# Kernel optimization log

Hardware: AMD Instinct MI355X
Metric: run time of the kernel (lower is better)

The kernel has to match this reference:

```python
import jax, jax.numpy as jnp
import numpy as np

N = 100000      # num nodes (single ntype)
D_IN = 256      # input_dim
D_OUT = 128     # output_dim (embedding_dim)
H = 4           # attn_heads
C = D_OUT // H  # out_channels per head
R = 3           # num metapaths with tail 'gene'; num_tail_relations = R + 1
E = 600000      # edges per metapath


def setup_inputs() -> dict:
    key = jax.random.key(0)
    ks = jax.random.split(key, 12)
    x = jax.random.normal(ks[0], (N, D_IN), dtype=jnp.float32)
    edge_index = jax.random.randint(ks[1], (R, 2, E), 0, N, dtype=jnp.int32)
    # per-ntype linear_l / linear_r (single ntype 'gene')
    sc = 1.0 / np.sqrt(D_IN)
    Wl = jax.random.normal(ks[2], (D_IN, D_OUT), dtype=jnp.float32) * sc
    bl = jnp.zeros((D_OUT,), dtype=jnp.float32)
    Wr = jax.random.normal(ks[3], (D_IN, D_OUT), dtype=jnp.float32) * sc
    br = jnp.zeros((D_OUT,), dtype=jnp.float32)
    # edge-level attention params: (R, H, 2C)
    attn = jax.random.normal(ks[4], (R, H, 2 * C), dtype=jnp.float32) * 0.1
    # relation-level attention params
    rel_attn_l = jax.random.normal(ks[5], (H, C), dtype=jnp.float32) * 0.1
    rel_attn_r = jax.random.normal(ks[6], (R + 1, H, C), dtype=jnp.float32) * 0.1
    rel_bias = jnp.zeros((R + 1,), dtype=jnp.float32)
    return {"x": x, "edge_index": edge_index, "Wl": Wl, "bl": bl, "Wr": Wr,
            "br": br, "attn": attn, "rel_attn_l": rel_attn_l,
            "rel_attn_r": rel_attn_r, "rel_bias": rel_bias}


def _segment_softmax(logits, seg, num_segments):
    # logits: (E, H), seg: (E,) dst ids -> softmax over edges sharing a dst
    m = jax.ops.segment_max(logits, seg, num_segments=num_segments)  # (N, H)
    e = jnp.exp(logits - m[seg])
    s = jax.ops.segment_sum(e, seg, num_segments=num_segments)       # (N, H)
    return e / (s[seg] + 1e-16)


def reference(x, edge_index, Wl, bl, Wr, br, attn, rel_attn_l, rel_attn_r, rel_bias):
    # projection: relu(Linear(x)).view(N, H, C)
    l = jax.nn.relu(x @ Wl + bl).reshape(N, H, C)
    r = jax.nn.relu(x @ Wr + br).reshape(N, H, C)

    def per_relation(ei, attn_m):
        src, dst = ei[0], ei[1]
        # alpha_e = LeakyReLU( l[src].attn_l + r[dst].attn_r ), per head
        a = (jnp.einsum('ehc,hc->eh', l[src], attn_m[:, :C])
             + jnp.einsum('ehc,hc->eh', r[dst], attn_m[:, C:]))  # (E, H)
        a = jax.nn.leaky_relu(a, negative_slope=0.2)
        alpha = _segment_softmax(a, dst, N)                      # (E, H)
        msg = l[src] * alpha[..., None]                          # (E, H, C)
        return jax.ops.segment_sum(msg, dst, num_segments=N)     # (N, H, C)

    emb_rel = jax.vmap(per_relation)(edge_index, attn)           # (R, N, H, C)
    # last relation slot is the self projection l
    emb = jnp.concatenate([jnp.moveaxis(emb_rel, 0, 1), l[:, None]], axis=1)  # (N, R+1, H, C)

    # relation-level beta attention
    beta_l = jax.nn.relu(r * rel_attn_l)                          # (N, H, C)
    beta_r = jax.nn.relu(emb * rel_attn_r)                        # (N, R+1, H, C)
    beta = jnp.einsum('nhc,nrhc->nrh', beta_l, beta_r) + rel_bias[None, :, None]
    beta = jax.nn.softmax(beta, axis=1)                           # (N, R+1, H)

    h = (emb * beta[..., None]).sum(axis=1).reshape(N, D_OUT)
    return jax.nn.relu(h)
```

## Files before the change

kernel.cpp:

```cpp
#include <hip/hip_runtime.h>
#include <hip/hip_bf16.h>

#define N_NODES 100000
#define N_EDGES 600000
#define N_REL   3
#define D_INF   256
#define D_OUTF  128
#define TOT_E   (3 * N_EDGES)

#define NB_REL   49
#define NBUCKT   (3 * NB_REL)
#define CAPB     16384

#define NPART_BLOCKS ((TOT_E + 4095) / 4096)

#define NPROJ_BLOCKS (((N_NODES + 63) / 64) * 2)
#define NTOT_BLOCKS  (NPROJ_BLOCKS + NBUCKT)

typedef __attribute__((ext_vector_type(8))) short          bf16x8;
typedef __attribute__((ext_vector_type(8))) unsigned short ushort8;
typedef __attribute__((ext_vector_type(4))) float          f32x4;

#define LPAD 72
#define LTS  136

__device__ __forceinline__ unsigned short bf16_rne(float v) {
    unsigned int b = __float_as_uint(v);
    b += 0x7FFFu + ((b >> 16) & 1u);
    return (unsigned short)(b >> 16);
}

__global__ __launch_bounds__(256) void part_wt(
    const float* __restrict__ Wl, const float* __restrict__ Wr,
    unsigned short* __restrict__ wt,
    const int* __restrict__ ei, int* __restrict__ bcnt,
    uint2* __restrict__ gstage)
{
    const int bid = blockIdx.x;
    const int t   = threadIdx.x;
    if (bid < 256) {
        const int k = bid;
        const int w = t >> 7;
        const int n = t & 127;
        const float v = (w ? Wr : Wl)[(size_t)k * D_OUTF + n];
        const unsigned short h = bf16_rne(v);
        const float fhi = __uint_as_float(((unsigned int)h) << 16);
        const unsigned short g = bf16_rne(v - fhi);
        const int kb   = k >> 6;
        const int kk   = (k >> 5) & 1;
        const int lgrp = (k >> 3) & 3;
        const int j    = k & 7;
        const int cf   = n >> 4;
        const int lane = lgrp * 16 + (n & 15);
        const size_t fh = ((((size_t)(w * 2 + 0) * 4 + kb) * 2 + kk) * 8 + cf) * 512 + lane * 8 + j;
        const size_t fl = ((((size_t)(w * 2 + 1) * 4 + kb) * 2 + kk) * 8 + cf) * 512 + lane * 8 + j;
        wt[fh] = h;
        wt[fl] = g;
        return;
    }
    __shared__ int lh[NBUCKT];
    __shared__ int lc[NBUCKT];
    const int base = (bid - 256) * 4096;

    for (int q = t; q < NBUCKT; q += 256) lh[q] = 0;
    __syncthreads();
#pragma unroll
    for (int r = 0; r < 16; ++r) {
        const int ge = base + r * 256 + t;
        if (ge < TOT_E) {
            const int rr = (ge >= 2 * N_EDGES) ? 2 : ((ge >= N_EDGES) ? 1 : 0);
            const int e  = ge - rr * N_EDGES;
            const int dst = ei[(size_t)rr * 2 * N_EDGES + N_EDGES + e];
            atomicAdd(&lh[rr * NB_REL + (dst >> 11)], 1);
        }
    }
    __syncthreads();
    for (int q = t; q < NBUCKT; q += 256)
        lc[q] = lh[q] ? atomicAdd(&bcnt[q], lh[q]) : 0;
    __syncthreads();
#pragma unroll
    for (int r = 0; r < 16; ++r) {
        const int ge = base + r * 256 + t;
        if (ge < TOT_E) {
            const int rr = (ge >= 2 * N_EDGES) ? 2 : ((ge >= N_EDGES) ? 1 : 0);
            const int e  = ge - rr * N_EDGES;
            const int src = ei[(size_t)rr * 2 * N_EDGES + e];
            const int dst = ei[(size_t)rr * 2 * N_EDGES + N_EDGES + e];
            const int qb  = rr * NB_REL + (dst >> 11);
            const int off = atomicAdd(&lc[qb], 1);
            uint2 u; u.x = (unsigned)src; u.y = (unsigned)(dst | (rr << 20));
            gstage[(size_t)qb * CAPB + off] = u;
        }
    }
}

__global__ __launch_bounds__(256, 6) void proj_scatter(
    const float* __restrict__ x, const unsigned short* __restrict__ wt,
    const float* __restrict__ bl, const float* __restrict__ br,
    const float* __restrict__ attn,
    float* __restrict__ rbuf,
    float* __restrict__ alr,  float* __restrict__ ar,
    unsigned short* __restrict__ lbf,
    const uint2* __restrict__ gstage, const int* __restrict__ bcnt,
    int* __restrict__ deg, int* __restrict__ rowst, int* __restrict__ colall)
{
    __shared__ unsigned short smem[2 * 64 * LPAD];
    __shared__ int wsum2[4];
    __shared__ int wexcl2[4];

    const int bid = blockIdx.x;
    const unsigned int pb = (unsigned int)(((unsigned long long)bid * NPROJ_BLOCKS) / NTOT_BLOCKS);
    const unsigned int pa = (unsigned int)(((unsigned long long)(bid + 1) * NPROJ_BLOCKS) / NTOT_BLOCKS);

    if (pa == pb) {
        const int b     = bid - (int)pb;
        const int rrb   = b / NB_REL;
        const int node0 = (b % NB_REL) * 2048;
        const int nN    = min(2048, N_NODES - node0);
        const int t     = threadIdx.x;
        int* hist = (int*)smem;
        const int cnt_b = bcnt[b];
        const size_t sbase = (size_t)b * CAPB;

        {
            int pv = (t < b) ? bcnt[t] : 0;
#pragma unroll
            for (int m = 32; m >= 1; m >>= 1) pv += __shfl_xor(pv, m);
            if ((t & 63) == 0) wsum2[t >> 6] = pv;
        }
        for (int q = t; q < 2048; q += 256) hist[q] = 0;
        __syncthreads();
        const int gb = wsum2[0] + wsum2[1] + wsum2[2] + wsum2[3];

        for (int e = t; e < cnt_b; e += 256) {
            const uint2 u = gstage[sbase + e];
            atomicAdd(&hist[(int)(u.y & 0xFFFFFu) - node0], 1);
        }
        __syncthreads();
        for (int q = t; q < nN; q += 256)
            deg[rrb * N_NODES + node0 + q] = hist[q];
        __syncthreads();
        {
            const int lane = t & 63;
            const int wid  = t >> 6;
            int v[8]; int tsum = 0;
#pragma unroll
            for (int i = 0; i < 8; ++i) { v[i] = hist[t * 8 + i]; tsum += v[i]; }
            int inc = tsum;
#pragma unroll
            for (int off2 = 1; off2 < 64; off2 <<= 1) {
                const int u2 = __shfl_up(inc, off2);
                if (lane >= off2) inc += u2;
            }
            if (lane == 63) wsum2[wid] = inc;
            __syncthreads();
            if (t == 0) {
                int s = 0;
#pragma unroll
                for (int i2 = 0; i2 < 4; ++i2) { const int tv = wsum2[i2]; wexcl2[i2] = s; s += tv; }
            }
            __syncthreads();
            int run = gb + wexcl2[wid] + (inc - tsum);
#pragma unroll
            for (int i = 0; i < 8; ++i) {
                const int q = t * 8 + i;
                const int st = run;
                run += v[i];
                hist[q] = st;
                if (q < nN) rowst[rrb * N_NODES + node0 + q] = st;
            }
        }
        __syncthreads();
        for (int e = t; e < cnt_b; e += 256) {
            const uint2 u = gstage[sbase + e];
            const int loc = (int)(u.y & 0xFFFFFu) - node0;
            const int pos = atomicAdd(&hist[loc], 1);
            colall[pos] = (int)u.x;
        }
        return;
    }

    const int tid  = threadIdx.x;
    const int nb   = (int)(pb >> 1) * 64;
    const int w    = (int)(pb & 1);

    const int lane = tid & 63;
    const int wv   = tid >> 6;
    const int rowf = lane & 15;
    const int kgrp = lane >> 4;

    f32x4 acc[8];
#pragma unroll
    for (int cf = 0; cf < 8; ++cf) acc[cf] = (f32x4){0.f, 0.f, 0.f, 0.f};

    for (int kb4 = 0; kb4 < 4; ++kb4) {
        __syncthreads();
        {
            const int r   = tid >> 2;
            const int seg = tid & 3;
            int rowg = nb + r; if (rowg >= N_NODES) rowg = N_NODES - 1;
            const float* src = x + (size_t)rowg * D_INF + kb4 * 64 + seg * 16;
#pragma unroll
            for (int q2 = 0; q2 < 2; ++q2) {
                const float4 v0 = *reinterpret_cast<const float4*>(src + q2 * 8);
                const float4 v1 = *reinterpret_cast<const float4*>(src + q2 * 8 + 4);
                const float vv[8] = {v0.x, v0.y, v0.z, v0.w, v1.x, v1.y, v1.z, v1.w};
                ushort8 hv, gv;
#pragma unroll
                for (int q = 0; q < 8; ++q) {
                    const unsigned short h = bf16_rne(vv[q]);
                    hv[q] = h;
                    const float fhi = __uint_as_float(((unsigned int)h) << 16);
                    gv[q] = bf16_rne(vv[q] - fhi);
                }
                *reinterpret_cast<ushort8*>(&smem[0 * 64 * LPAD + r * LPAD + seg * 16 + q2 * 8]) = hv;
                *reinterpret_cast<ushort8*>(&smem[1 * 64 * LPAD + r * LPAD + seg * 16 + q2 * 8]) = gv;
            }
        }
        __syncthreads();

#pragma unroll
        for (int kk = 0; kk < 2; ++kk) {
            const int ko = kk * 32 + kgrp * 8;
            const bf16x8 ahi = *reinterpret_cast<const bf16x8*>(&smem[0 * 64 * LPAD + (wv * 16 + rowf) * LPAD + ko]);
            const bf16x8 alo = *reinterpret_cast<const bf16x8*>(&smem[1 * 64 * LPAD + (wv * 16 + rowf) * LPAD + ko]);
#pragma unroll
            for (int cf = 0; cf < 8; ++cf) {
                const bf16x8 bhi = *reinterpret_cast<const bf16x8*>(
                    wt + ((((size_t)(w * 2 + 0) * 4 + kb4) * 2 + kk) * 8 + cf) * 512 + lane * 8);
                const bf16x8 blo = *reinterpret_cast<const bf16x8*>(
                    wt + ((((size_t)(w * 2 + 1) * 4 + kb4) * 2 + kk) * 8 + cf) * 512 + lane * 8);
                acc[cf] = __builtin_amdgcn_mfma_f32_16x16x32_bf16(ahi, bhi, acc[cf], 0, 0, 0);
                acc[cf] = __builtin_amdgcn_mfma_f32_16x16x32_bf16(ahi, blo, acc[cf], 0, 0, 0);
                acc[cf] = __builtin_amdgcn_mfma_f32_16x16x32_bf16(alo, bhi, acc[cf], 0, 0, 0);
            }
        }
    }
    __syncthreads();

    float o_[8][4];
    {
        const float* bias = w ? br : bl;
#pragma unroll
        for (int cf = 0; cf < 8; ++cf) {
            const float bvv = bias[cf * 16 + rowf];
#pragma unroll
            for (int j = 0; j < 4; ++j)
                o_[cf][j] = fmaxf(acc[cf][j] + bvv, 0.f);
        }
    }

    if (w == 1) {
#pragma unroll
        for (int cf = 0; cf < 8; ++cf)
#pragma unroll
            for (int j = 0; j < 4; ++j) {
                const int node = nb + wv * 16 + kgrp * 4 + j;
                if (node < N_NODES)
                    rbuf[(size_t)node * D_OUTF + cf * 16 + rowf] = o_[cf][j];
            }
    }

    {
        const int woff = w ? 32 : 0;
#pragma unroll
        for (int rr = 0; rr < 3; ++rr) {
            float pr[4][4];
#pragma unroll
            for (int hh = 0; hh < 4; ++hh) {
                const float A0 = attn[rr * 256 + hh * 64 + woff + rowf];
                const float A1 = attn[rr * 256 + hh * 64 + woff + 16 + rowf];
#pragma unroll
                for (int j = 0; j < 4; ++j)
                    pr[hh][j] = fmaf(o_[2 * hh][j], A0, o_[2 * hh + 1][j] * A1);
            }
#pragma unroll
            for (int hh = 0; hh < 4; ++hh)
#pragma unroll
                for (int j = 0; j < 4; ++j) {
#pragma unroll
                    for (int m = 8; m >= 1; m >>= 1)
                        pr[hh][j] += __shfl_xor(pr[hh][j], m);
                }
            if ((rowf >> 2) == rr) {
#pragma unroll
                for (int j = 0; j < 4; ++j) {
                    float v = pr[0][j];
#pragma unroll
                    for (int hh = 1; hh < 4; ++hh)
                        if ((rowf & 3) == hh) v = pr[hh][j];
                    const int node = nb + wv * 16 + kgrp * 4 + j;
                    if (node < N_NODES) {
                        if (w == 0)
                            alr[((size_t)rr * N_NODES + node) * 4 + (rowf & 3)] = v;
                        else
                            ar[(size_t)node * 12 + rowf] = v;
                    }
                }
            }
        }
    }

    if (w == 0) {
#pragma unroll
        for (int cf = 0; cf < 8; ++cf)
#pragma unroll
            for (int j = 0; j < 4; ++j)
                smem[(wv * 16 + kgrp * 4 + j) * LTS + cf * 16 + rowf] = bf16_rne(o_[cf][j]);
        __syncthreads();
#pragma unroll
        for (int q = 0; q < 4; ++q) {
            const int idx = tid + q * 256;
            const int r2  = idx >> 4;
            const int c8  = (idx & 15) * 8;
            const int node = nb + r2;
            if (node < N_NODES)
                *reinterpret_cast<ushort8*>(&lbf[(size_t)node * D_OUTF + c8]) =
                    *reinterpret_cast<ushort8*>(&smem[r2 * LTS + c8]);
        }
    }
}

__global__ __launch_bounds__(256) void aggregate_kernel(
    const uint4* __restrict__ lbf128, const float* __restrict__ rbuf,
    const float* __restrict__ alr,  const float* __restrict__ ar,
    const int* __restrict__ rowst,  const int* __restrict__ deg,
    const int* __restrict__ colall,
    const float* __restrict__ rel_attn_l, const float* __restrict__ rel_attn_r,
    const float* __restrict__ rel_bias,   float* __restrict__ out)
{
    __shared__ int   src_sh[4][4][3][16];
    __shared__ float w_sh[4][4][3][16][4];

    const int wv   = threadIdx.x >> 6;
    const int lane = threadIdx.x & 63;
    const int g    = lane >> 4;
    const int j    = lane & 15;
    const int n    = blockIdx.x * 16 + wv * 4 + g;

    const int h  = j >> 2;
    const int c8 = j * 8;

    int   start_[3], cnt_[3], cm_[3], base_[3];
    float4 ar4_[3];
#pragma unroll
    for (int rr = 0; rr < 3; ++rr) {
        start_[rr] = rowst[rr * N_NODES + n];
        cnt_[rr]   = deg[rr * N_NODES + n];
        ar4_[rr]   = *reinterpret_cast<const float4*>(ar + (size_t)n * 12 + rr * 4);
        int cm = cnt_[rr];
        cm = max(cm, __shfl_xor(cm, 16));
        cm = max(cm, __shfl_xor(cm, 32));
        cm_[rr] = cm;
        base_[rr] = 0;
    }

    float ex[3][8];
    float den[3];
#pragma unroll
    for (int rr = 0; rr < 3; ++rr) {
        den[rr] = 0.f;
#pragma unroll
        for (int c = 0; c < 8; ++c) ex[rr][c] = 0.f;
    }

    while (base_[0] < cm_[0] || base_[1] < cm_[1] || base_[2] < cm_[2]) {
        int mm_[3];
        int mxw_[3];
#pragma unroll
        for (int rr = 0; rr < 3; ++rr) {
            mm_[rr] = 0; mxw_[rr] = 0;
            if (base_[rr] < cm_[rr]) {
                mm_[rr]  = min(16, max(0, cnt_[rr] - base_[rr]));
                mxw_[rr] = min(16, cm_[rr] - base_[rr]);
                const int sj = (j < mm_[rr]) ? colall[start_[rr] + base_[rr] + j] : 0;
                const float4 al4 = *reinterpret_cast<const float4*>(
                    alr + ((size_t)rr * N_NODES + sj) * 4);
                float t0 = al4.x + ar4_[rr].x, t1 = al4.y + ar4_[rr].y;
                float t2 = al4.z + ar4_[rr].z, t3 = al4.w + ar4_[rr].w;
                t0 = fmaxf(t0, 0.2f * t0); t1 = fmaxf(t1, 0.2f * t1);
                t2 = fmaxf(t2, 0.2f * t2); t3 = fmaxf(t3, 0.2f * t3);
                float e0 = __expf(t0), e1 = __expf(t1);
                float e2 = __expf(t2), e3 = __expf(t3);
                if (j >= mm_[rr]) { e0 = 0.f; e1 = 0.f; e2 = 0.f; e3 = 0.f; }
                src_sh[wv][g][rr][j] = sj;
                f32x4 w4; w4[0] = e0; w4[1] = e1; w4[2] = e2; w4[3] = e3;
                *reinterpret_cast<f32x4*>(&w_sh[wv][g][rr][j][0]) = w4;
            }
        }
        const int mxall = max(mxw_[0], max(mxw_[1], mxw_[2]));
        for (int i = 0; i < mxall; ++i) {
#pragma unroll
            for (int rr = 0; rr < 3; ++rr) {
                if (i < mm_[rr]) {
                    const int   srcI = src_sh[wv][g][rr][i];
                    const float wsel = w_sh[wv][g][rr][i][h];
                    const uint4 u = lbf128[(size_t)srcI * 16 + j];
                    den[rr] += wsel;
                    ex[rr][0] = fmaf(wsel, __uint_as_float(u.x << 16),         ex[rr][0]);
                    ex[rr][1] = fmaf(wsel, __uint_as_float(u.x & 0xFFFF0000u), ex[rr][1]);
                    ex[rr][2] = fmaf(wsel, __uint_as_float(u.y << 16),         ex[rr][2]);
                    ex[rr][3] = fmaf(wsel, __uint_as_float(u.y & 0xFFFF0000u), ex[rr][3]);
                    ex[rr][4] = fmaf(wsel, __uint_as_float(u.z << 16),         ex[rr][4]);
                    ex[rr][5] = fmaf(wsel, __uint_as_float(u.z & 0xFFFF0000u), ex[rr][5]);
                    ex[rr][6] = fmaf(wsel, __uint_as_float(u.w << 16),         ex[rr][6]);
                    ex[rr][7] = fmaf(wsel, __uint_as_float(u.w & 0xFFFF0000u), ex[rr][7]);
                }
            }
        }
#pragma unroll
        for (int rr = 0; rr < 3; ++rr) base_[rr] += 16;
    }

    float e[4][8];
#pragma unroll
    for (int rr = 0; rr < 3; ++rr) {
        const float inv = 1.f / (den[rr] + 1e-16f);
#pragma unroll
        for (int c = 0; c < 8; ++c) e[rr][c] = ex[rr][c] * inv;
    }
    {
        const uint4 u = lbf128[(size_t)n * 16 + j];
        e[3][0] = __uint_as_float(u.x << 16);
        e[3][1] = __uint_as_float(u.x & 0xFFFF0000u);
        e[3][2] = __uint_as_float(u.y << 16);
        e[3][3] = __uint_as_float(u.y & 0xFFFF0000u);
        e[3][4] = __uint_as_float(u.z << 16);
        e[3][5] = __uint_as_float(u.z & 0xFFFF0000u);
        e[3][6] = __uint_as_float(u.w << 16);
        e[3][7] = __uint_as_float(u.w & 0xFFFF0000u);
    }

    float blc[8];
    {
        const float4 rva = *reinterpret_cast<const float4*>(rbuf + (size_t)n * D_OUTF + c8);
        const float4 rvb = *reinterpret_cast<const float4*>(rbuf + (size_t)n * D_OUTF + c8 + 4);
        const float4 rla = *reinterpret_cast<const float4*>(rel_attn_l + c8);
        const float4 rlb = *reinterpret_cast<const float4*>(rel_attn_l + c8 + 4);
        blc[0] = fmaxf(rva.x * rla.x, 0.f);
        blc[1] = fmaxf(rva.y * rla.y, 0.f);
        blc[2] = fmaxf(rva.z * rla.z, 0.f);
        blc[3] = fmaxf(rva.w * rla.w, 0.f);
        blc[4] = fmaxf(rvb.x * rlb.x, 0.f);
        blc[5] = fmaxf(rvb.y * rlb.y, 0.f);
        blc[6] = fmaxf(rvb.z * rlb.z, 0.f);
        blc[7] = fmaxf(rvb.w * rlb.w, 0.f);
    }

    float beta[4];
#pragma unroll
    for (int s = 0; s < 4; ++s) {
        const float4 ra = *reinterpret_cast<const float4*>(rel_attn_r + s * D_OUTF + c8);
        const float4 rb = *reinterpret_cast<const float4*>(rel_attn_r + s * D_OUTF + c8 + 4);
        float p = 0.f;
        p = fmaf(blc[0], fmaxf(e[s][0] * ra.x, 0.f), p);
        p = fmaf(blc[1], fmaxf(e[s][1] * ra.y, 0.f), p);
        p = fmaf(blc[2], fmaxf(e[s][2] * ra.z, 0.f), p);
        p = fmaf(blc[3], fmaxf(e[s][3] * ra.w, 0.f), p);
        p = fmaf(blc[4], fmaxf(e[s][4] * rb.x, 0.f), p);
        p = fmaf(blc[5], fmaxf(e[s][5] * rb.y, 0.f), p);
        p = fmaf(blc[6], fmaxf(e[s][6] * rb.z, 0.f), p);
        p = fmaf(blc[7], fmaxf(e[s][7] * rb.w, 0.f), p);
        p += __shfl_xor(p, 2);
        p += __shfl_xor(p, 1);
        beta[s] = p + rel_bias[s];
    }

    const float mx2 = fmaxf(fmaxf(beta[0], beta[1]), fmaxf(beta[2], beta[3]));
    float ssum = 0.f;
#pragma unroll
    for (int s = 0; s < 4; ++s) { beta[s] = __expf(beta[s] - mx2); ssum += beta[s]; }
    const float isum = 1.f / ssum;
    float o[8];
#pragma unroll
    for (int c = 0; c < 8; ++c) o[c] = 0.f;
#pragma unroll
    for (int s = 0; s < 4; ++s) {
        const float b = beta[s] * isum;
#pragma unroll
        for (int c = 0; c < 8; ++c) o[c] = fmaf(e[s][c], b, o[c]);
    }
    float4 ova, ovb;
    ova.x = fmaxf(o[0], 0.f); ova.y = fmaxf(o[1], 0.f);
    ova.z = fmaxf(o[2], 0.f); ova.w = fmaxf(o[3], 0.f);
    ovb.x = fmaxf(o[4], 0.f); ovb.y = fmaxf(o[5], 0.f);
    ovb.z = fmaxf(o[6], 0.f); ovb.w = fmaxf(o[7], 0.f);
    *reinterpret_cast<float4*>(out + (size_t)n * D_OUTF + c8)     = ova;
    *reinterpret_cast<float4*>(out + (size_t)n * D_OUTF + c8 + 4) = ovb;
}

extern "C" void kernel_launch(void* const* d_in, const int* in_sizes, int n_in,
                              void* d_out, int out_size, void* d_ws, size_t ws_size,
                              hipStream_t stream)
{
    const float* x     = (const float*)d_in[0];
    const int*   ei    = (const int*)  d_in[1];
    const float* Wl    = (const float*)d_in[2];
    const float* bl    = (const float*)d_in[3];
    const float* Wr    = (const float*)d_in[4];
    const float* br    = (const float*)d_in[5];
    const float* attn  = (const float*)d_in[6];
    const float* ral   = (const float*)d_in[7];
    const float* rar   = (const float*)d_in[8];
    const float* rbias = (const float*)d_in[9];
    float* out = (float*)d_out;

    char* ws = (char*)d_ws;
    size_t off = 0;
    float* rbuf   = (float*)(ws + off); off += (size_t)N_NODES * D_OUTF * 4;
    float* alr    = (float*)(ws + off); off += (size_t)3 * N_NODES * 4 * 4;
    float* ar     = (float*)(ws + off); off += (size_t)N_NODES * 12 * 4;
    int*   deg    = (int*)  (ws + off); off += (size_t)3 * N_NODES * 4;
    int*   rowst  = (int*)  (ws + off); off += (size_t)3 * N_NODES * 4;
    int*   colall = (int*)  (ws + off); off += (size_t)TOT_E * 4;
    int*   bcnt   = (int*)  (ws + off); off += (size_t)256 * 4;
    unsigned short* wt  = (unsigned short*)(ws + off); off += (size_t)2 * 2 * 128 * 256 * 2;
    unsigned short* lbf = (unsigned short*)(ws + off); off += (size_t)N_NODES * D_OUTF * 2;
    uint2* gstage = (uint2*)(ws + off); off += (size_t)NBUCKT * CAPB * 8;

    hipMemsetAsync(bcnt, 0, (size_t)NBUCKT * 4, stream);

    part_wt<<<256 + NPART_BLOCKS, 256, 0, stream>>>(Wl, Wr, wt, ei, bcnt, gstage);

    proj_scatter<<<NTOT_BLOCKS, 256, 0, stream>>>(
        x, wt, bl, br, attn, rbuf, alr, ar, lbf, gstage, bcnt,
        deg, rowst, colall);

    aggregate_kernel<<<N_NODES / 16, 256, 0, stream>>>(
        (const uint4*)lbf, rbuf, alr, ar, rowst, deg, colall,
        ral, rar, rbias, out);
}
```

Before: 257.9 us.

## Merge Wl and Wr projection halves into one 512-thread block per node tile

Each projection block now runs 512 threads (8 waves): four waves compute the Wl half and four the Wr half for the same 64-node tile. Before, two separate 256-thread blocks each did one half. The x tile is loaded from global memory and split into hi/lo bf16 once and shared by both halves, which halves the x reads and the conversion work. The CSR scatter-partition path is adapted to 512 threads with 4 elements per thread in the scan. The cost is larger blocks, more barrier coupling and a tighter register budget from launch_bounds(512,8).

Measured after the change: 288.9 us. 1.12x slower.

```diff
diff --git a/kernel.cpp b/kernel.cpp
--- a/kernel.cpp
+++ b/kernel.cpp
@@ -14,7 +14,7 @@
 
 #define NPART_BLOCKS ((TOT_E + 4095) / 4096)
 
-#define NPROJ_BLOCKS (((N_NODES + 63) / 64) * 2)
+#define NPROJ_BLOCKS ((N_NODES + 63) / 64)
 #define NTOT_BLOCKS  (NPROJ_BLOCKS + NBUCKT)
 
 typedef __attribute__((ext_vector_type(8))) short          bf16x8;
@@ -94,7 +94,7 @@
     }
 }
 
-__global__ __launch_bounds__(256, 6) void proj_scatter(
+__global__ __launch_bounds__(512, 8) void proj_scatter(
     const float* __restrict__ x, const unsigned short* __restrict__ wt,
     const float* __restrict__ bl, const float* __restrict__ br,
     const float* __restrict__ attn,
@@ -105,8 +105,8 @@
     int* __restrict__ deg, int* __restrict__ rowst, int* __restrict__ colall)
 {
     __shared__ unsigned short smem[2 * 64 * LPAD];
-    __shared__ int wsum2[4];
-    __shared__ int wexcl2[4];
+    __shared__ int wsum2[8];
+    __shared__ int wexcl2[8];
 
     const int bid = blockIdx.x;
     const unsigned int pb = (unsigned int)(((unsigned long long)bid * NPROJ_BLOCKS) / NTOT_BLOCKS);
@@ -128,24 +128,26 @@
             for (int m = 32; m >= 1; m >>= 1) pv += __shfl_xor(pv, m);
             if ((t & 63) == 0) wsum2[t >> 6] = pv;
         }
-        for (int q = t; q < 2048; q += 256) hist[q] = 0;
+        for (int q = t; q < 2048; q += 512) hist[q] = 0;
         __syncthreads();
-        const int gb = wsum2[0] + wsum2[1] + wsum2[2] + wsum2[3];
-
-        for (int e = t; e < cnt_b; e += 256) {
+        int gb = 0;
+#pragma unroll
+        for (int i = 0; i < 8; ++i) gb += wsum2[i];
+
+        for (int e = t; e < cnt_b; e += 512) {
             const uint2 u = gstage[sbase + e];
             atomicAdd(&hist[(int)(u.y & 0xFFFFFu) - node0], 1);
         }
         __syncthreads();
-        for (int q = t; q < nN; q += 256)
+        for (int q = t; q < nN; q += 512)
             deg[rrb * N_NODES + node0 + q] = hist[q];
         __syncthreads();
         {
             const int lane = t & 63;
             const int wid  = t >> 6;
-            int v[8]; int tsum = 0;
-#pragma unroll
-            for (int i = 0; i < 8; ++i) { v[i] = hist[t * 8 + i]; tsum += v[i]; }
+            int v[4]; int tsum = 0;
+#pragma unroll
+            for (int i = 0; i < 4; ++i) { v[i] = hist[t * 4 + i]; tsum += v[i]; }
             int inc = tsum;
 #pragma unroll
             for (int off2 = 1; off2 < 64; off2 <<= 1) {
@@ -157,13 +159,13 @@
             if (t == 0) {
                 int s = 0;
 #pragma unroll
-                for (int i2 = 0; i2 < 4; ++i2) { const int tv = wsum2[i2]; wexcl2[i2] = s; s += tv; }
+                for (int i2 = 0; i2 < 8; ++i2) { const int tv = wsum2[i2]; wexcl2[i2] = s; s += tv; }
             }
             __syncthreads();
             int run = gb + wexcl2[wid] + (inc - tsum);
 #pragma unroll
-            for (int i = 0; i < 8; ++i) {
-                const int q = t * 8 + i;
+            for (int i = 0; i < 4; ++i) {
+                const int q = t * 4 + i;
                 const int st = run;
                 run += v[i];
                 hist[q] = st;
@@ -171,7 +173,7 @@
             }
         }
         __syncthreads();
-        for (int e = t; e < cnt_b; e += 256) {
+        for (int e = t; e < cnt_b; e += 512) {
             const uint2 u = gstage[sbase + e];
             const int loc = (int)(u.y & 0xFFFFFu) - node0;
             const int pos = atomicAdd(&hist[loc], 1);
@@ -181,13 +183,19 @@
     }
 
     const int tid  = threadIdx.x;
-    const int nb   = (int)(pb >> 1) * 64;
-    const int w    = (int)(pb & 1);
+    const int nb   = (int)pb * 64;
 
     const int lane = tid & 63;
-    const int wv   = tid >> 6;
+    const int wave = tid >> 6;
+    const int w    = wave >> 2;
+    const int wv   = wave & 3;
     const int rowf = lane & 15;
     const int kgrp = lane >> 4;
+
+    const int r_   = tid >> 3;
+    const int seg_ = tid & 7;
+    int rowg = nb + r_; if (rowg >= N_NODES) rowg = N_NODES - 1;
+    const float* xrow = x + (size_t)rowg * D_INF + seg_ * 8;
 
     f32x4 acc[8];
 #pragma unroll
@@ -196,26 +204,20 @@
     for (int kb4 = 0; kb4 < 4; ++kb4) {
         __syncthreads();
         {
-            const int r   = tid >> 2;
-            const int seg = tid & 3;
-            int rowg = nb + r; if (rowg >= N_NODES) rowg = N_NODES - 1;
-            const float* src = x + (size_t)rowg * D_INF + kb4 * 64 + seg * 16;
-#pragma unroll
-            for (int q2 = 0; q2 < 2; ++q2) {
-                const float4 v0 = *reinterpret_cast<const float4*>(src + q2 * 8);
-                const float4 v1 = *reinterpret_cast<const float4*>(src + q2 * 8 + 4);
-                const float vv[8] = {v0.x, v0.y, v0.z, v0.w, v1.x, v1.y, v1.z, v1.w};
-                ushort8 hv, gv;
-#pragma unroll
-                for (int q = 0; q < 8; ++q) {
-                    const unsigned short h = bf16_rne(vv[q]);
-                    hv[q] = h;
-                    const float fhi = __uint_as_float(((unsigned int)h) << 16);
-                    gv[q] = bf16_rne(vv[q] - fhi);
-                }
-                *reinterpret_cast<ushort8*>(&smem[0 * 64 * LPAD + r * LPAD + seg * 16 + q2 * 8]) = hv;
-                *reinterpret_cast<ushort8*>(&smem[1 * 64 * LPAD + r * LPAD + seg * 16 + q2 * 8]) = gv;
-            }
+            const float* s = xrow + kb4 * 64;
+            const float4 v0 = *reinterpret_cast<const float4*>(s);
+            const float4 v1 = *reinterpret_cast<const float4*>(s + 4);
+            const float vv[8] = {v0.x, v0.y, v0.z, v0.w, v1.x, v1.y, v1.z, v1.w};
+            ushort8 hv, gv;
+#pragma unroll
+            for (int q = 0; q < 8; ++q) {
+                const unsigned short h = bf16_rne(vv[q]);
+                hv[q] = h;
+                const float fhi = __uint_as_float(((unsigned int)h) << 16);
+                gv[q] = bf16_rne(vv[q] - fhi);
+            }
+            *reinterpret_cast<ushort8*>(&smem[0 * 64 * LPAD + r_ * LPAD + seg_ * 8]) = hv;
+            *reinterpret_cast<ushort8*>(&smem[1 * 64 * LPAD + r_ * LPAD + seg_ * 8]) = gv;
         }
         __syncthreads();
 
@@ -307,17 +309,17 @@
 #pragma unroll
             for (int j = 0; j < 4; ++j)
                 smem[(wv * 16 + kgrp * 4 + j) * LTS + cf * 16 + rowf] = bf16_rne(o_[cf][j]);
-        __syncthreads();
-#pragma unroll
-        for (int q = 0; q < 4; ++q) {
-            const int idx = tid + q * 256;
-            const int r2  = idx >> 4;
-            const int c8  = (idx & 15) * 8;
-            const int node = nb + r2;
-            if (node < N_NODES)
-                *reinterpret_cast<ushort8*>(&lbf[(size_t)node * D_OUTF + c8]) =
-                    *reinterpret_cast<ushort8*>(&smem[r2 * LTS + c8]);
-        }
+    }
+    __syncthreads();
+#pragma unroll
+    for (int q = 0; q < 2; ++q) {
+        const int idx = tid + q * 512;
+        const int r2  = idx >> 4;
+        const int c8  = (idx & 15) * 8;
+        const int node = nb + r2;
+        if (node < N_NODES)
+            *reinterpret_cast<ushort8*>(&lbf[(size_t)node * D_OUTF + c8]) =
+                *reinterpret_cast<ushort8*>(&smem[r2 * LTS + c8]);
     }
 }
 
@@ -522,7 +524,7 @@
 
     part_wt<<<256 + NPART_BLOCKS, 256, 0, stream>>>(Wl, Wr, wt, ei, bcnt, gstage);
 
-    proj_scatter<<<NTOT_BLOCKS, 256, 0, stream>>>(
+    proj_scatter<<<NTOT_BLOCKS, 512, 0, stream>>>(
         x, wt, bl, br, attn, rbuf, alr, ar, lbf, gstage, bcnt,
         deg, rowst, colall);
 
```
